# Kernel optimization log

Measured on AMD Instinct MI355X. Metric: run time of the kernel, lower is better.

The kernel has to match this reference:

```python
import jax, jax.numpy as jnp
import numpy as np

EPS = 1e-5


def setup_inputs() -> dict:
    key = jax.random.key(0)
    ks = jax.random.split(key, 8)
    Ns, E, F, H, O = 8192, 200000, 20, 1024, 2
    N = Ns + E
    return {
        "state": jax.random.normal(ks[0], (Ns, F), dtype=jnp.float32),
        "edge_attr": jax.random.normal(ks[1], (E, F), dtype=jnp.float32),
        "edge_index": jax.random.randint(ks[2], (2, E), 0, N, dtype=jnp.int64),
        "W_gcn": jax.random.normal(ks[3], (F, H), dtype=jnp.float32) * 0.05,
        "b_gcn": jax.random.normal(ks[4], (H,), dtype=jnp.float32) * 0.05,
        "gamma": jnp.ones((H,), dtype=jnp.float32),
        "beta": jnp.zeros((H,), dtype=jnp.float32),
        "W_lin": jax.random.normal(ks[5], (H, O), dtype=jnp.float32) * 0.05,
        "b_lin": jnp.zeros((O,), dtype=jnp.float32),
    }


def gcn_conv(x, edge_index, W, b):
    # PyG GCNConv: add self-loops, symmetric deg^{-1/2} normalization,
    # linear transform, sum-aggregate src -> dst, add bias.
    N = x.shape[0]
    loop = jnp.arange(N, dtype=edge_index.dtype)
    src = jnp.concatenate([edge_index[0], loop])
    dst = jnp.concatenate([edge_index[1], loop])
    deg = jnp.zeros((N,), dtype=x.dtype).at[dst].add(1.0)  # >=1 from self-loops
    dinv = jax.lax.rsqrt(deg)
    norm = dinv[src] * dinv[dst]                 # [E+N]
    xw = x @ W                                   # [N, H]
    msg = xw[src] * norm[:, None]                # [E+N, H] gather + scale
    out = jax.ops.segment_sum(msg, dst, num_segments=N)  # scatter-add
    return out + b


def reference(state, edge_attr, edge_index, W_gcn, b_gcn, gamma, beta, W_lin, b_lin):
    # node features = cat(state, edge_attr) along node dim
    node_features = jnp.concatenate([state, edge_attr], axis=0)  # [N, 20]
    h = gcn_conv(node_features, edge_index, W_gcn, b_gcn)        # [N, 1024]
    # BatchNorm1d (train-mode: batch statistics, biased variance)
    mean = jnp.mean(h, axis=0)
    var = jnp.mean(jnp.square(h - mean), axis=0)
    h = (h - mean) * jax.lax.rsqrt(var + EPS) * gamma + beta
    # Linear -> ReLU -> Softmax(dim=1)
    logits = jax.nn.relu(h @ W_lin + b_lin)                      # [N, 2]
    return jax.nn.softmax(logits, axis=1)
```

## Files before the change

kernel.cpp:

```cpp
#include <hip/hip_runtime.h>


#define F 20
#define NSTAT 230
#define SROWS 256
#define BSZ 256
#define TBSZ 512
#define CPAD 32

__global__ void k_init(float* __restrict__ deg, float* __restrict__ stats, int N) {
  int i = blockIdx.x * blockDim.x + threadIdx.x;
  if (i < N) deg[i] = 0.f;
  if (i < 256) stats[i] = 0.f;
}

__global__ void k_deg_acc(const int* __restrict__ dst, float* __restrict__ deg, int E) {
  int e = blockIdx.x * blockDim.x + threadIdx.x;
  if (e < E) atomicAdd(&deg[dst[e]], 1.0f);
}

__global__ __launch_bounds__(BSZ) void k_counts(const float* __restrict__ deg,
                                                int* __restrict__ counts, int N) {
  __shared__ float s[BSZ];
  int t = threadIdx.x;
  long row = (long)blockIdx.x * SROWS + t;
  s[t] = (row < N) ? deg[row] : 0.f;
  __syncthreads();
  for (int off = 128; off; off >>= 1) {
    if (t < off) s[t] += s[t + off];
    __syncthreads();
  }
  if (t == 0) counts[blockIdx.x] = (int)(s[0] + 0.5f);
}

__global__ __launch_bounds__(1024) void k_scan(const int* __restrict__ counts,
                                               int* __restrict__ bstart,
                                               int* __restrict__ cursor,
                                               int NB, int E) {
  __shared__ int s[1024];
  int t = threadIdx.x;
  int c = (t < NB) ? counts[t] : 0;
  s[t] = c;
  __syncthreads();
  for (int off = 1; off < 1024; off <<= 1) {
    int v = (t >= off) ? s[t - off] : 0;
    __syncthreads();
    s[t] += v;
    __syncthreads();
  }
  if (t < NB) {
    int excl = s[t] - c;
    bstart[t] = excl;
    cursor[t * CPAD] = excl;
  }
  if (t == 0) bstart[NB] = E;
}

__global__ void k_fill(const int* __restrict__ src, const int* __restrict__ dst,
                       const float* __restrict__ deg, int* __restrict__ cursor,
                       uint2* __restrict__ erec8, int E) {
  int e = blockIdx.x * blockDim.x + threadIdx.x;
  if (e >= E) return;
  int s = src[e];
  int d = dst[e];
  int pos = atomicAdd(&cursor[(d >> 8) * CPAD], 1);
  uint2 r;
  r.x = (unsigned int)s | ((unsigned int)(d & 255) << 22);
  r.y = __float_as_uint(rsqrtf(deg[s] + 1.0f));
  erec8[pos] = r;
}

__global__ __launch_bounds__(TBSZ) void k_tile(
    const uint2* __restrict__ erec8, const int* __restrict__ bstart,
    const float* __restrict__ deg,
    const float* __restrict__ state, const float* __restrict__ edge_attr,
    float* __restrict__ y, float* __restrict__ stats, int N, int Ns) {
  __shared__ float tile[SROWS * F];
  __shared__ float pp[2][NSTAT];
  int t = threadIdx.x;

  for (int i4 = t; i4 < SROWS * 5; i4 += TBSZ)
    *reinterpret_cast<float4*>(tile + i4 * 4) = make_float4(0.f, 0.f, 0.f, 0.f);
  __syncthreads();

  int start = bstart[blockIdx.x];
  int cnt = bstart[blockIdx.x + 1] - start;
  int sb = Ns * F;
  int nit = cnt * F;
  for (int it0 = t; it0 < nit; it0 += 4 * TBSZ) {
    float val[4];
    int ad[4];
    bool on[4];
    #pragma unroll
    for (int u = 0; u < 4; ++u) {
      int it = it0 + u * TBSZ;
      on[u] = (it < nit);
      val[u] = 0.f;
      ad[u] = 0;
      if (on[u]) {
        int le = it / F;
        int f = it - le * F;
        uint2 r = erec8[start + le];
        int s = r.x & 0x3FFFFF;
        int dlow = r.x >> 22;
        float ns = __uint_as_float(r.y);
        int xi = s * F + f;
        float x = (xi < sb) ? state[xi] : edge_attr[xi - sb];
        val[u] = ns * x;
        ad[u] = dlow * F + f;
      }
    }
    #pragma unroll
    for (int u = 0; u < 4; ++u)
      if (on[u]) atomicAdd(&tile[ad[u]], val[u]);
  }
  __syncthreads();

  long rowbase = (long)blockIdx.x * SROWS;
  for (int i4 = t; i4 < SROWS * 5; i4 += TBSZ) {
    int rl = i4 / 5;
    int q = i4 - rl * 5;
    long row = rowbase + rl;
    float4 v = make_float4(0.f, 0.f, 0.f, 0.f);
    if (row < N) {
      float4 zv = *reinterpret_cast<const float4*>(tile + i4 * 4);
      const float* xrow = (row < (long)Ns) ? (state + row * F)
                                           : (edge_attr + (row - Ns) * F);
      float4 xv = *reinterpret_cast<const float4*>(xrow + q * 4);
      float di = rsqrtf(deg[row] + 1.0f);
      v.x = di * (zv.x + di * xv.x);
      v.y = di * (zv.y + di * xv.y);
      v.z = di * (zv.z + di * xv.z);
      v.w = di * (zv.w + di * xv.w);
      *reinterpret_cast<float4*>(y + row * F + q * 4) = v;
    }
    *reinterpret_cast<float4*>(tile + i4 * 4) = v;
  }
  __syncthreads();

  int g = t >> 8;
  int c = t & 255;
  int r0 = g * 128;
  if (c < F) {
    float a0 = 0.f, a1 = 0.f, a2 = 0.f, a3 = 0.f;
    for (int r = r0; r < r0 + 128; r += 4) {
      a0 += tile[(r + 0) * F + c];
      a1 += tile[(r + 1) * F + c];
      a2 += tile[(r + 2) * F + c];
      a3 += tile[(r + 3) * F + c];
    }
    pp[g][c] = (a0 + a1) + (a2 + a3);
  } else if (c < NSTAT) {
    int k = c - F, i = 0;
    while (k >= F - i) { k -= F - i; i++; }
    int ci = i, cj = i + k;
    float a0 = 0.f, a1 = 0.f, a2 = 0.f, a3 = 0.f;
    for (int r = r0; r < r0 + 128; r += 4) {
      a0 += tile[(r + 0) * F + ci] * tile[(r + 0) * F + cj];
      a1 += tile[(r + 1) * F + ci] * tile[(r + 1) * F + cj];
      a2 += tile[(r + 2) * F + ci] * tile[(r + 2) * F + cj];
      a3 += tile[(r + 3) * F + ci] * tile[(r + 3) * F + cj];
    }
    pp[g][c] = (a0 + a1) + (a2 + a3);
  }
  __syncthreads();
  if (t < NSTAT) atomicAdd(&stats[t], pp[0][t] + pp[1][t]);
}

__global__ __launch_bounds__(256, 1) void k_finalize(
    const float* __restrict__ stats,
    const float* __restrict__ W_gcn,
    const float* __restrict__ gamma,
    const float* __restrict__ beta,
    const float* __restrict__ W_lin,
    const float* __restrict__ b_lin,
    float* __restrict__ params,
    int N, int H) {
  __shared__ float Cu_s[210];
  __shared__ float ybar_s[F];
  __shared__ float part[4][44];
  int t = threadIdx.x;
  int lane = t & 63;
  int wv = t >> 6;
  float invN = 1.0f / (float)N;
  if (t < F) ybar_s[t] = stats[t] * invN;
  __syncthreads();
  if (t < 210) {
    int k = t, i = 0;
    while (k >= F - i) { k -= F - i; i++; }
    int j = i + k;
    float cv = stats[F + t] * invN - ybar_s[i] * ybar_s[j];
    Cu_s[t] = (i == j) ? cv : 2.0f * cv;
  }
  __syncthreads();

  float m0[F], m1[F];
  #pragma unroll
  for (int f = 0; f < F; ++f) { m0[f] = 0.f; m1[f] = 0.f; }
  float d0 = 0.f, d1 = 0.f;

  for (int hb = 0; hb < H; hb += 4 * 256) {
    float w[4][F];
    float var[4];
    int hh[4];
    bool act[4];
    #pragma unroll
    for (int c = 0; c < 4; ++c) {
      int h = hb + c * 256 + t;
      act[c] = (h < H);
      hh[c] = act[c] ? h : 0;
      var[c] = 0.f;
      #pragma unroll
      for (int f = 0; f < F; ++f) {
        float x = W_gcn[f * H + hh[c]];
        w[c][f] = act[c] ? x : 0.f;
      }
    }
    int p = 0;
    #pragma unroll
    for (int i = 0; i < F; ++i) {
      #pragma unroll
      for (int j = i; j < F; ++j) {
        float cu = Cu_s[p];
        ++p;
        #pragma unroll
        for (int c = 0; c < 4; ++c) var[c] += cu * (w[c][i] * w[c][j]);
      }
    }
    #pragma unroll
    for (int c = 0; c < 4; ++c) {
      float sg = act[c] ? (gamma[hh[c]] * rsqrtf(var[c] + 1e-5f)) : 0.f;
      float wl0 = W_lin[hh[c] * 2 + 0], wl1 = W_lin[hh[c] * 2 + 1];
      float s0 = sg * wl0, s1 = sg * wl1;
      #pragma unroll
      for (int f = 0; f < F; ++f) { m0[f] += w[c][f] * s0; m1[f] += w[c][f] * s1; }
      float bt = act[c] ? beta[hh[c]] : 0.f;
      d0 += bt * wl0;
      d1 += bt * wl1;
    }
  }

  #pragma unroll
  for (int f = 0; f < F; ++f) {
    float v0 = m0[f], v1 = m1[f];
    #pragma unroll
    for (int off = 32; off; off >>= 1) {
      v0 += __shfl_xor(v0, off);
      v1 += __shfl_xor(v1, off);
    }
    if (lane == 0) { part[wv][2 * f] = v0; part[wv][2 * f + 1] = v1; }
  }
  #pragma unroll
  for (int off = 32; off; off >>= 1) {
    d0 += __shfl_xor(d0, off);
    d1 += __shfl_xor(d1, off);
  }
  if (lane == 0) { part[wv][40] = d0; part[wv][41] = d1; }
  __syncthreads();

  if (t < 42) {
    float acc = 0.f;
    for (int w2 = 0; w2 < 4; ++w2) acc += part[w2][t];
    if (t >= 40) acc += b_lin[t - 40];
    params[t] = acc;
  } else if (t < 62) {
    params[t] = ybar_s[t - 42];
  }
}

__global__ void k_out(const float* __restrict__ y,
                      const float* __restrict__ params,
                      float* __restrict__ out, int N) {
  __shared__ float P[64];
  if (threadIdx.x < 62) P[threadIdx.x] = params[threadIdx.x];
  __syncthreads();
  int n = blockIdx.x * blockDim.x + threadIdx.x;
  if (n >= N) return;
  const float4* yr4 = reinterpret_cast<const float4*>(y + (size_t)n * F);
  float l0 = P[40], l1 = P[41];
  #pragma unroll
  for (int k = 0; k < 5; ++k) {
    float4 q = yr4[k];
    float vv[4] = {q.x, q.y, q.z, q.w};
    #pragma unroll
    for (int u = 0; u < 4; ++u) {
      int f = 4 * k + u;
      float dv = vv[u] - P[42 + f];
      l0 += dv * P[2 * f + 0];
      l1 += dv * P[2 * f + 1];
    }
  }
  l0 = fmaxf(l0, 0.f);
  l1 = fmaxf(l1, 0.f);
  float m = fmaxf(l0, l1);
  float e0 = __expf(l0 - m), e1 = __expf(l1 - m);
  float inv = 1.0f / (e0 + e1);
  float2 o2;
  o2.x = e0 * inv;
  o2.y = e1 * inv;
  reinterpret_cast<float2*>(out)[n] = o2;
}

extern "C" void kernel_launch(void* const* d_in, const int* in_sizes, int n_in,
                              void* d_out, int out_size, void* d_ws, size_t ws_size,
                              hipStream_t stream) {
  const float* state     = (const float*)d_in[0];
  const float* edge_attr = (const float*)d_in[1];
  const int*   eidx      = (const int*)d_in[2];
  const float* W_gcn     = (const float*)d_in[3];
  const float* gamma     = (const float*)d_in[5];
  const float* beta      = (const float*)d_in[6];
  const float* W_lin     = (const float*)d_in[7];
  const float* b_lin     = (const float*)d_in[8];
  float* out = (float*)d_out;

  int Ns = in_sizes[0] / F;
  int E  = in_sizes[2] / 2;
  int N  = Ns + in_sizes[1] / F;
  int H  = in_sizes[4];

  const int* src = eidx;
  const int* dst = eidx + E;

  int NB = (N + SROWS - 1) / SROWS;

  float* ws     = (float*)d_ws;
  float* deg    = ws;
  float* y      = ws + N;
  float* stats  = y + (size_t)N * F;
  float* params = stats + 256;
  int*   counts = (int*)(params + 64);
  int*   bstart = counts + NB;
  int*   cursor = bstart + NB + 1;
  uint2* erec8  = (uint2*)(cursor + NB * CPAD);

  k_init<<<(N + BSZ - 1) / BSZ, BSZ, 0, stream>>>(deg, stats, N);
  k_deg_acc<<<(E + BSZ - 1) / BSZ, BSZ, 0, stream>>>(dst, deg, E);
  k_counts<<<NB, BSZ, 0, stream>>>(deg, counts, N);
  k_scan<<<1, 1024, 0, stream>>>(counts, bstart, cursor, NB, E);
  k_fill<<<(E + BSZ - 1) / BSZ, BSZ, 0, stream>>>(src, dst, deg, cursor,
                                                  erec8, E);
  k_tile<<<NB, TBSZ, 0, stream>>>(erec8, bstart, deg, state, edge_attr,
                                  y, stats, N, Ns);
  k_finalize<<<1, 256, 0, stream>>>(stats, W_gcn, gamma, beta, W_lin, b_lin,
                                    params, N, H);
  k_out<<<(N + BSZ - 1) / BSZ, BSZ, 0, stream>>>(y, params, out, N);
}
```

Before: 110.8 us.

## Halve tile rows per block, spread stats atomics over 8 copies

Shrinks each destination tile from 256 to 128 rows with 256-thread blocks, which doubles the block count so the GPU gets more parallelism and less shared-memory atomic contention per block. The scan now handles two counts per thread so the block count can grow past 1024, and the bucket encoding is adjusted to 7 bits. Global stats accumulation is split across 8 replicated copies, summed in finalize, to reduce atomic contention on 230 addresses. The edge loop's 4x unroll is dropped, which may reduce memory-level parallelism per thread.

Result: faster. 94.91 us (-14.3%).

```diff
diff --git a/kernel.cpp b/kernel.cpp
--- a/kernel.cpp
+++ b/kernel.cpp
@@ -3,15 +3,15 @@
 
 #define F 20
 #define NSTAT 230
-#define SROWS 256
+#define SROWS 128
 #define BSZ 256
-#define TBSZ 512
+#define TBSZ 256
 #define CPAD 32
 
 __global__ void k_init(float* __restrict__ deg, float* __restrict__ stats, int N) {
   int i = blockIdx.x * blockDim.x + threadIdx.x;
   if (i < N) deg[i] = 0.f;
-  if (i < 256) stats[i] = 0.f;
+  if (i < 8 * 256) stats[i] = 0.f;
 }
 
 __global__ void k_deg_acc(const int* __restrict__ dst, float* __restrict__ deg, int E) {
@@ -19,14 +19,14 @@
   if (e < E) atomicAdd(&deg[dst[e]], 1.0f);
 }
 
-__global__ __launch_bounds__(BSZ) void k_counts(const float* __restrict__ deg,
+__global__ __launch_bounds__(128) void k_counts(const float* __restrict__ deg,
                                                 int* __restrict__ counts, int N) {
-  __shared__ float s[BSZ];
+  __shared__ float s[128];
   int t = threadIdx.x;
   long row = (long)blockIdx.x * SROWS + t;
   s[t] = (row < N) ? deg[row] : 0.f;
   __syncthreads();
-  for (int off = 128; off; off >>= 1) {
+  for (int off = 64; off; off >>= 1) {
     if (t < off) s[t] += s[t + off];
     __syncthreads();
   }
@@ -39,8 +39,11 @@
                                                int NB, int E) {
   __shared__ int s[1024];
   int t = threadIdx.x;
-  int c = (t < NB) ? counts[t] : 0;
-  s[t] = c;
+  int i0 = 2 * t, i1 = 2 * t + 1;
+  int c0 = (i0 < NB) ? counts[i0] : 0;
+  int c1 = (i1 < NB) ? counts[i1] : 0;
+  int sum = c0 + c1;
+  s[t] = sum;
   __syncthreads();
   for (int off = 1; off < 1024; off <<= 1) {
     int v = (t >= off) ? s[t - off] : 0;
@@ -48,11 +51,9 @@
     s[t] += v;
     __syncthreads();
   }
-  if (t < NB) {
-    int excl = s[t] - c;
-    bstart[t] = excl;
-    cursor[t * CPAD] = excl;
-  }
+  int base = s[t] - sum;
+  if (i0 < NB) { bstart[i0] = base;      cursor[i0 * CPAD] = base; }
+  if (i1 < NB) { bstart[i1] = base + c0; cursor[i1 * CPAD] = base + c0; }
   if (t == 0) bstart[NB] = E;
 }
 
@@ -63,9 +64,9 @@
   if (e >= E) return;
   int s = src[e];
   int d = dst[e];
-  int pos = atomicAdd(&cursor[(d >> 8) * CPAD], 1);
+  int pos = atomicAdd(&cursor[(d >> 7) * CPAD], 1);
   uint2 r;
-  r.x = (unsigned int)s | ((unsigned int)(d & 255) << 22);
+  r.x = (unsigned int)s | ((unsigned int)(d & 127) << 22);
   r.y = __float_as_uint(rsqrtf(deg[s] + 1.0f));
   erec8[pos] = r;
 }
@@ -76,7 +77,6 @@
     const float* __restrict__ state, const float* __restrict__ edge_attr,
     float* __restrict__ y, float* __restrict__ stats, int N, int Ns) {
   __shared__ float tile[SROWS * F];
-  __shared__ float pp[2][NSTAT];
   int t = threadIdx.x;
 
   for (int i4 = t; i4 < SROWS * 5; i4 += TBSZ)
@@ -87,32 +87,16 @@
   int cnt = bstart[blockIdx.x + 1] - start;
   int sb = Ns * F;
   int nit = cnt * F;
-  for (int it0 = t; it0 < nit; it0 += 4 * TBSZ) {
-    float val[4];
-    int ad[4];
-    bool on[4];
-    #pragma unroll
-    for (int u = 0; u < 4; ++u) {
-      int it = it0 + u * TBSZ;
-      on[u] = (it < nit);
-      val[u] = 0.f;
-      ad[u] = 0;
-      if (on[u]) {
-        int le = it / F;
-        int f = it - le * F;
-        uint2 r = erec8[start + le];
-        int s = r.x & 0x3FFFFF;
-        int dlow = r.x >> 22;
-        float ns = __uint_as_float(r.y);
-        int xi = s * F + f;
-        float x = (xi < sb) ? state[xi] : edge_attr[xi - sb];
-        val[u] = ns * x;
-        ad[u] = dlow * F + f;
-      }
-    }
-    #pragma unroll
-    for (int u = 0; u < 4; ++u)
-      if (on[u]) atomicAdd(&tile[ad[u]], val[u]);
+  for (int it = t; it < nit; it += TBSZ) {
+    int le = it / F;
+    int f = it - le * F;
+    uint2 r = erec8[start + le];
+    int s = r.x & 0x3FFFFF;
+    int dlow = r.x >> 22;
+    float ns = __uint_as_float(r.y);
+    int xi = s * F + f;
+    float x = (xi < sb) ? state[xi] : edge_attr[xi - sb];
+    atomicAdd(&tile[dlow * F + f], ns * x);
   }
   __syncthreads();
 
@@ -138,33 +122,29 @@
   }
   __syncthreads();
 
-  int g = t >> 8;
-  int c = t & 255;
-  int r0 = g * 128;
-  if (c < F) {
+  float* st = stats + (blockIdx.x & 7) * 256;
+  if (t < F) {
     float a0 = 0.f, a1 = 0.f, a2 = 0.f, a3 = 0.f;
-    for (int r = r0; r < r0 + 128; r += 4) {
-      a0 += tile[(r + 0) * F + c];
-      a1 += tile[(r + 1) * F + c];
-      a2 += tile[(r + 2) * F + c];
-      a3 += tile[(r + 3) * F + c];
-    }
-    pp[g][c] = (a0 + a1) + (a2 + a3);
-  } else if (c < NSTAT) {
-    int k = c - F, i = 0;
+    for (int r = 0; r < SROWS; r += 4) {
+      a0 += tile[(r + 0) * F + t];
+      a1 += tile[(r + 1) * F + t];
+      a2 += tile[(r + 2) * F + t];
+      a3 += tile[(r + 3) * F + t];
+    }
+    atomicAdd(&st[t], (a0 + a1) + (a2 + a3));
+  } else if (t < NSTAT) {
+    int k = t - F, i = 0;
     while (k >= F - i) { k -= F - i; i++; }
     int ci = i, cj = i + k;
     float a0 = 0.f, a1 = 0.f, a2 = 0.f, a3 = 0.f;
-    for (int r = r0; r < r0 + 128; r += 4) {
+    for (int r = 0; r < SROWS; r += 4) {
       a0 += tile[(r + 0) * F + ci] * tile[(r + 0) * F + cj];
       a1 += tile[(r + 1) * F + ci] * tile[(r + 1) * F + cj];
       a2 += tile[(r + 2) * F + ci] * tile[(r + 2) * F + cj];
       a3 += tile[(r + 3) * F + ci] * tile[(r + 3) * F + cj];
     }
-    pp[g][c] = (a0 + a1) + (a2 + a3);
-  }
-  __syncthreads();
-  if (t < NSTAT) atomicAdd(&stats[t], pp[0][t] + pp[1][t]);
+    atomicAdd(&st[t], (a0 + a1) + (a2 + a3));
+  }
 }
 
 __global__ __launch_bounds__(256, 1) void k_finalize(
@@ -183,13 +163,19 @@
   int lane = t & 63;
   int wv = t >> 6;
   float invN = 1.0f / (float)N;
-  if (t < F) ybar_s[t] = stats[t] * invN;
+  if (t < F) {
+    float s = 0.f;
+    for (int k = 0; k < 8; ++k) s += stats[k * 256 + t];
+    ybar_s[t] = s * invN;
+  }
   __syncthreads();
   if (t < 210) {
     int k = t, i = 0;
     while (k >= F - i) { k -= F - i; i++; }
     int j = i + k;
-    float cv = stats[F + t] * invN - ybar_s[i] * ybar_s[j];
+    float sv = 0.f;
+    for (int c = 0; c < 8; ++c) sv += stats[c * 256 + F + t];
+    float cv = sv * invN - ybar_s[i] * ybar_s[j];
     Cu_s[t] = (i == j) ? cv : 2.0f * cv;
   }
   __syncthreads();
@@ -328,7 +314,7 @@
   float* deg    = ws;
   float* y      = ws + N;
   float* stats  = y + (size_t)N * F;
-  float* params = stats + 256;
+  float* params = stats + 8 * 256;
   int*   counts = (int*)(params + 64);
   int*   bstart = counts + NB;
   int*   cursor = bstart + NB + 1;
@@ -336,7 +322,7 @@
 
   k_init<<<(N + BSZ - 1) / BSZ, BSZ, 0, stream>>>(deg, stats, N);
   k_deg_acc<<<(E + BSZ - 1) / BSZ, BSZ, 0, stream>>>(dst, deg, E);
-  k_counts<<<NB, BSZ, 0, stream>>>(deg, counts, N);
+  k_counts<<<NB, 128, 0, stream>>>(deg, counts, N);
   k_scan<<<1, 1024, 0, stream>>>(counts, bstart, cursor, NB, E);
   k_fill<<<(E + BSZ - 1) / BSZ, BSZ, 0, stream>>>(src, dst, deg, cursor,
                                                   erec8, E);
```
